# Kernel tuning notes

Hardware: AMD Instinct MI355X
Metric: run time of the kernel (lower is better)

Reference implementation:

```python
import jax, jax.numpy as jnp
import numpy as np

D_MODEL = 768
BATCH = 2
N_CTX = 4096


def setup_inputs() -> dict:
    key = jax.random.key(0)
    k1, k2 = jax.random.split(key)
    x = jax.random.normal(k1, (BATCH, N_CTX, D_MODEL), dtype=jnp.float32)
    # proj: Linear(d_model, 3*d_model, bias=False); torch stores weight as [out, in]
    W_proj = jax.random.normal(k2, (3 * D_MODEL, D_MODEL), dtype=jnp.float32) * (1.0 / np.sqrt(D_MODEL))
    return {"x": x, "W_proj": W_proj}


def reference(x, W_proj):
    d = x.shape[-1]
    n_ctx = x.shape[-2]
    # qkv: [B, S, 3D] = x @ W^T (torch Linear semantics)
    qkv = jnp.einsum("bsd,ed->bse", x, W_proj)
    Q, K, V = jnp.split(qkv, 3, axis=-1)
    # additive causal mask: 0 on/below diagonal, -inf above (1 - 1/tril(ones))
    causal = jnp.tril(jnp.ones((n_ctx, n_ctx), dtype=bool))
    mask = jnp.where(causal, 0.0, -jnp.inf).astype(x.dtype)
    # NOTE: no 1/sqrt(d) scaling in the original module
    scores = jnp.einsum("bqd,bkd->bqk", Q, K) + mask
    attn = jax.nn.softmax(scores, axis=-1)
    out = x + jnp.einsum("bqk,bkd->bqd", attn, V)
    return out
```

## Files before the change

### kernel.cpp

```cpp
#include <hip/hip_runtime.h>
#include <hip/hip_bf16.h>
#include <hip/hip_fp16.h>

typedef _Float16 f16;
typedef _Float16 f16x8 __attribute__((ext_vector_type(8)));
typedef _Float16 f16x4 __attribute__((ext_vector_type(4)));
typedef _Float16 f16x2 __attribute__((ext_vector_type(2)));
typedef float f32x4 __attribute__((ext_vector_type(4)));

#define D_MODEL 768
#define S_CTX   4096
#define NBATCH  2
#define M_TOK   (NBATCH * S_CTX)
#define N3      (3 * D_MODEL)

__device__ __forceinline__ void gload_lds16(const void* g, void* l) {
  __builtin_amdgcn_global_load_lds(
      (__attribute__((address_space(1))) unsigned int*)g,
      (__attribute__((address_space(3))) unsigned int*)l, 16, 0, 0);
}

__global__ __launch_bounds__(256) void cvt_f32_f16(const float* __restrict__ s,
                                                   f16* __restrict__ d, int n4) {
  int i = blockIdx.x * 256 + threadIdx.x;
  if (i >= n4) return;
  f32x4 v = ((const f32x4*)s)[i];
  f16x4 h;
  h[0] = (f16)v[0]; h[1] = (f16)v[1]; h[2] = (f16)v[2]; h[3] = (f16)v[3];
  ((f16x4*)d)[i] = h;
}

__global__ __launch_bounds__(256, 2) void proj_gemm(
    const f16* __restrict__ A, const f16* __restrict__ B,
    f16* __restrict__ qh, f16* __restrict__ kh, f16* __restrict__ vth) {
  __shared__ f16 As[128 * 32];
  __shared__ f16 Bs[128 * 32];

  const int tid  = threadIdx.x;
  const int w    = tid >> 6, lane = tid & 63;
  const int wr   = w >> 1,   wc   = w & 1;
  const int bm0  = blockIdx.x * 128, bn0 = blockIdx.y * 128;
  const int srow = lane >> 2;
  const int scol = (lane & 3) * 8;

  f32x4 acc[4][4] = {};

  const f16* gA = A + (size_t)bm0 * 768;
  const f16* gB = B + (size_t)bn0 * 768;

  for (int kt = 0; kt < 24; ++kt) {
    __syncthreads();
    const int k0 = kt * 32 + scol;
#pragma unroll
    for (int cc = 0; cc < 2; ++cc) {
      int c = w + cc * 4;
      gload_lds16(gA + (size_t)(c * 16 + srow) * 768 + k0, (char*)As + c * 1024);
      gload_lds16(gB + (size_t)(c * 16 + srow) * 768 + k0, (char*)Bs + c * 1024);
    }
    __syncthreads();

    const int fr = lane & 15, fk = (lane >> 4) * 8;
    f16x8 af[4], bf[4];
#pragma unroll
    for (int i = 0; i < 4; ++i)
      af[i] = *(const f16x8*)(As + (wr * 64 + i * 16 + fr) * 32 + fk);
#pragma unroll
    for (int j = 0; j < 4; ++j)
      bf[j] = *(const f16x8*)(Bs + (wc * 64 + j * 16 + fr) * 32 + fk);
#pragma unroll
    for (int i = 0; i < 4; ++i)
#pragma unroll
      for (int j = 0; j < 4; ++j)
        acc[i][j] = __builtin_amdgcn_mfma_f32_16x16x32_f16(af[i], bf[j], acc[i][j], 0, 0, 0);
  }

  const int fr = lane & 15, fq = lane >> 4;
#pragma unroll
  for (int i = 0; i < 4; ++i) {
#pragma unroll
    for (int j = 0; j < 4; ++j) {
      int gn      = bn0 + wc * 64 + j * 16 + fr;
      int gm_base = bm0 + wr * 64 + i * 16 + fq * 4;
      if (gn < 1536) {
        f16* dst = (gn < 768) ? qh : kh;
        int  col = (gn < 768) ? gn : gn - 768;
#pragma unroll
        for (int r = 0; r < 4; ++r)
          dst[(size_t)(gm_base + r) * 768 + col] = (f16)acc[i][j][r];
      } else {
        int d = gn - 1536;
        int bb = gm_base >> 12, s = gm_base & 4095;
        f16x4 h;
        h[0] = (f16)acc[i][j][0]; h[1] = (f16)acc[i][j][1];
        h[2] = (f16)acc[i][j][2]; h[3] = (f16)acc[i][j][3];
        *(f16x4*)(vth + ((size_t)bb * 768 + d) * 4096 + s) = h;
      }
    }
  }
}

#define SM_K0   0
#define SM_K1   49152
#define SM_SS   98304
#define SM_PS   106496
#define SM_M    108544
#define SM_L    108672
#define SM_F    108800
#define SM_SZ   108928

__global__ __launch_bounds__(512, 2) void attn_part(
    const f16* __restrict__ qg, const f16* __restrict__ kg,
    const f16* __restrict__ vt, f16* __restrict__ p0,
    float* __restrict__ p1, float* __restrict__ ml) {
  extern __shared__ __align__(16) char smem[];
  char*  Kb0 = smem + SM_K0;
  char*  Kb1 = smem + SM_K1;
  float* Ss0 = (float*)(smem + SM_SS);
  float* Ss1 = Ss0 + 1024;
  char*  Ps  = smem + SM_PS;
  float* mS  = (float*)(smem + SM_M);
  float* lS  = (float*)(smem + SM_L);
  float* fS  = (float*)(smem + SM_F);

  const int tid  = threadIdx.x;
  const int wv   = tid >> 6, lane = tid & 63;
  const int fr   = lane & 15, fq = lane >> 4;
  const int qi   = wv >> 2, ki = (wv >> 1) & 1, dh = wv & 1;

  const int u = blockIdx.x;
  int vv = (u < 256) ? u : (u - 256);
  const int qb = ((u < 256) ? 127 : 63) - (vv >> 2);
  const int b  = (vv >> 1) & 1;
  const int c  = vv & 1;
  const int q0 = qb * 32;
  const int n  = (q0 >> 5) + 1;
  const int n0 = (n + 1) >> 1;
  const int ts = c ? n0 : 0;
  const int te = c ? n : n0;

  const char* kbase = (const char*)(kg + (size_t)b * 4096 * 768);
  const f16*  vbase = vt + (size_t)b * 768 * 4096;
  const f16*  vp0   = vbase + (size_t)(wv * 96 + fr) * 4096 + fq * 8;

  f16x8 qreg[12];
  {
    const f16* qp = qg + ((size_t)b * 4096 + q0 + qi * 16 + fr) * 768 + dh * 384 + fq * 8;
#pragma unroll
    for (int kk = 0; kk < 12; ++kk) qreg[kk] = *(const f16x8*)(qp + kk * 32);
  }

  if (tid < 32) { mS[tid] = -1e30f; lS[tid] = 0.f; }

  f32x4 acc[2][6] = {};

  if (ts < te) {
    const char* kb = kbase + (size_t)(ts * 32) * 1536;
    char* dst = (ts & 1) ? Kb1 : Kb0;
#pragma unroll
    for (int i = 0; i < 6; ++i) {
      int lin = wv * 6144 + i * 1024 + lane * 16;
      int row = lin / 1536, cb = lin - row * 1536;
      gload_lds16(kb + (size_t)row * 1536 + (cb ^ ((row & 7) << 4)),
                  dst + wv * 6144 + i * 1024);
    }
  }
  asm volatile("s_waitcnt vmcnt(0)" ::: "memory");
  __builtin_amdgcn_s_barrier();

  for (int t = ts; t < te; ++t) {
    const int kv0 = t * 32;
    const bool pf = (t + 1 < te);

    f16x8 vreg[6];
    {
      const f16* vp = vp0 + kv0;
#pragma unroll
      for (int ct = 0; ct < 6; ++ct)
        vreg[ct] = *(const f16x8*)(vp + (size_t)ct * 16 * 4096);
    }
    if (pf) {
      const char* kb = kbase + (size_t)(kv0 + 32) * 1536;
      char* dst = ((t + 1) & 1) ? Kb1 : Kb0;
#pragma unroll
      for (int i = 0; i < 6; ++i) {
        int lin = wv * 6144 + i * 1024 + lane * 16;
        int row = lin / 1536, cb = lin - row * 1536;
        gload_lds16(kb + (size_t)row * 1536 + (cb ^ ((row & 7) << 4)),
                    dst + wv * 6144 + i * 1024);
      }
    }

    {
      const char* kbuf = (t & 1) ? Kb1 : Kb0;
      f32x4 sc = {};
      const int krow = ki * 16 + fr;
      const int kswz = (krow & 7) << 4;
      __builtin_amdgcn_s_setprio(1);
#pragma unroll
      for (int kk = 0; kk < 12; ++kk) {
        int by = krow * 1536 + dh * 768 + kk * 64 + fq * 16;
        f16x8 kf = *(const f16x8*)(kbuf + (by ^ kswz));
        sc = __builtin_amdgcn_mfma_f32_16x16x32_f16(qreg[kk], kf, sc, 0, 0, 0);
      }
      __builtin_amdgcn_s_setprio(0);
      float* sdst = (dh ? Ss1 : Ss0) + (qi * 16 + fq * 4) * 32 + ki * 16 + fr;
#pragma unroll
      for (int r = 0; r < 4; ++r) sdst[r * 32] = sc[r];
    }
    asm volatile("s_waitcnt lgkmcnt(0)" ::: "memory");
    __builtin_amdgcn_s_barrier();

    {
      const int row = tid >> 4, sub = tid & 15;
      const int c0 = sub * 2;
      float a0 = Ss0[row * 32 + c0]     + Ss1[row * 32 + c0];
      float a1 = Ss0[row * 32 + c0 + 1] + Ss1[row * 32 + c0 + 1];
      const int grow = q0 + row;
      if (kv0 + c0     > grow) a0 = -1e30f;
      if (kv0 + c0 + 1 > grow) a1 = -1e30f;
      float mx = fmaxf(a0, a1);
      mx = fmaxf(mx, __shfl_xor(mx, 1));
      mx = fmaxf(mx, __shfl_xor(mx, 2));
      mx = fmaxf(mx, __shfl_xor(mx, 4));
      mx = fmaxf(mx, __shfl_xor(mx, 8));
      float mo = mS[row];
      float mn = fmaxf(mo, mx);
      float p0v = __expf(a0 - mn), p1v = __expf(a1 - mn);
      float sum = p0v + p1v;
      sum += __shfl_xor(sum, 1);
      sum += __shfl_xor(sum, 2);
      sum += __shfl_xor(sum, 4);
      sum += __shfl_xor(sum, 8);
      if (sub == 0) {
        float f = __expf(mo - mn);
        mS[row] = mn; fS[row] = f; lS[row] = lS[row] * f + sum;
      }
      f16x2 ph; ph[0] = (f16)p0v; ph[1] = (f16)p1v;
      int by = row * 64 + sub * 4;
      *(f16x2*)(Ps + (by ^ (((row >> 1) & 3) << 4))) = ph;
    }
    asm volatile("s_waitcnt lgkmcnt(0)" ::: "memory");
    __builtin_amdgcn_s_barrier();

    {
      f32x4 f0 = *(const f32x4*)(fS + fq * 4);
      f32x4 f1 = *(const f32x4*)(fS + 16 + fq * 4);
#pragma unroll
      for (int ct = 0; ct < 6; ++ct)
#pragma unroll
        for (int r = 0; r < 4; ++r) {
          acc[0][ct][r] *= f0[r];
          acc[1][ct][r] *= f1[r];
        }
      int byA0 = (fr * 64 + fq * 16) ^ (((fr >> 1) & 3) << 4);
      int rb = 16 + fr;
      int byA1 = (rb * 64 + fq * 16) ^ (((rb >> 1) & 3) << 4);
      f16x8 pa0 = *(const f16x8*)(Ps + byA0);
      f16x8 pa1 = *(const f16x8*)(Ps + byA1);
      __builtin_amdgcn_s_setprio(1);
#pragma unroll
      for (int ct = 0; ct < 6; ++ct) {
        acc[0][ct] = __builtin_amdgcn_mfma_f32_16x16x32_f16(pa0, vreg[ct], acc[0][ct], 0, 0, 0);
        acc[1][ct] = __builtin_amdgcn_mfma_f32_16x16x32_f16(pa1, vreg[ct], acc[1][ct], 0, 0, 0);
      }
      __builtin_amdgcn_s_setprio(0);
    }
    asm volatile("s_waitcnt vmcnt(0) lgkmcnt(0)" ::: "memory");
    __builtin_amdgcn_s_barrier();
  }

  const size_t obase = (size_t)b * 4096 + q0;
  if (c == 0) {
#pragma unroll
    for (int ct = 0; ct < 6; ++ct) {
      int d = wv * 96 + ct * 16 + fr;
#pragma unroll
      for (int r = 0; r < 4; ++r) {
        p0[(obase + fq * 4 + r) * 768 + d]      = (f16)acc[0][ct][r];
        p0[(obase + 16 + fq * 4 + r) * 768 + d] = (f16)acc[1][ct][r];
      }
    }
  } else {
#pragma unroll
    for (int ct = 0; ct < 6; ++ct) {
      int d = wv * 96 + ct * 16 + fr;
#pragma unroll
      for (int r = 0; r < 4; ++r) {
        p1[(obase + fq * 4 + r) * 768 + d]      = acc[0][ct][r];
        p1[(obase + 16 + fq * 4 + r) * 768 + d] = acc[1][ct][r];
      }
    }
  }
  if (tid < 32) {
    float* mlp = ml + ((size_t)(c * 2 + b) * 4096 + q0 + tid) * 2;
    mlp[0] = mS[tid];
    mlp[1] = lS[tid];
  }
}

__global__ __launch_bounds__(256) void attn_combine(
    const float* __restrict__ x, const f16* __restrict__ p0,
    const float* __restrict__ ml, float* __restrict__ out) {
  int i = blockIdx.x * 256 + threadIdx.x;
  int row = i / 192;
  int b = row >> 12, s = row & 4095;
  const float* m0p = ml + ((size_t)b * 4096 + s) * 2;
  const float* m1p = ml + ((size_t)(2 + b) * 4096 + s) * 2;
  float m0 = m0p[0], l0 = m0p[1];
  float m1 = m1p[0], l1 = m1p[1];
  float m  = fmaxf(m0, m1);
  float f0 = __expf(m0 - m), f1 = __expf(m1 - m);
  float inv = 1.f / (l0 * f0 + l1 * f1);
  f32x4 a1 = ((const f32x4*)out)[i];
  f16x4 a0 = ((const f16x4*)p0)[i];
  f32x4 xv = ((const f32x4*)x)[i];
  f32x4 o;
#pragma unroll
  for (int r = 0; r < 4; ++r)
    o[r] = xv[r] + ((float)a0[r] * f0 + a1[r] * f1) * inv;
  ((f32x4*)out)[i] = o;
}

extern "C" void kernel_launch(void* const* d_in, const int* in_sizes, int n_in,
                              void* d_out, int out_size, void* d_ws, size_t ws_size,
                              hipStream_t stream) {
  const float* x  = (const float*)d_in[0];
  const float* Wp = (const float*)d_in[1];
  float* out = (float*)d_out;

  char* ws = (char*)d_ws;
  f16* x_h  = (f16*)(ws);
  f16* w_h  = (f16*)(ws + 12582912);
  f16* q_h  = (f16*)(ws + 16121856);
  f16* k_h  = (f16*)(ws + 28704768);
  f16* vt_h = (f16*)(ws + 41287680);

  f16*   p0 = x_h;
  float* ml = (float*)w_h;

  hipFuncSetAttribute(reinterpret_cast<const void*>(attn_part),
                      hipFuncAttributeMaxDynamicSharedMemorySize, SM_SZ);

  cvt_f32_f16<<<(M_TOK * D_MODEL) / 1024, 256, 0, stream>>>(x, x_h, (M_TOK * D_MODEL) / 4);
  cvt_f32_f16<<<(N3 * D_MODEL) / 1024, 256, 0, stream>>>(Wp, w_h, (N3 * D_MODEL) / 4);
  proj_gemm<<<dim3(64, 18), 256, 0, stream>>>(x_h, w_h, q_h, k_h, vt_h);
  attn_part<<<512, 512, SM_SZ, stream>>>(q_h, k_h, vt_h, p0, out, ml);
  attn_combine<<<(M_TOK * D_MODEL) / 1024, 256, 0, stream>>>(x, p0, ml, out);
}
```

Before: 284.2 us.

## Single-buffer K tile in LDS to allow four workgroups per CU

Replaces the double-buffered K tile with a single LDS buffer, roughly halving shared memory per block, and raises the launch-bounds occupancy hint from 2 to 4 blocks. The prefetch of the next K tile is now issued after the score barrier, so it overlaps only the softmax and PV phase rather than the whole iteration. The aim is to hide latency through more resident blocks instead of intra-block double buffering. The risks are register spilling under the tighter launch bound and less overlap within each block. A redundant reload of the current tile is issued on the last iteration.

```diff
diff --git a/kernel.cpp b/kernel.cpp
--- a/kernel.cpp
+++ b/kernel.cpp
@@ -99,22 +99,20 @@
   }
 }
 
-#define SM_K0   0
-#define SM_K1   49152
-#define SM_SS   98304
-#define SM_PS   106496
-#define SM_M    108544
-#define SM_L    108672
-#define SM_F    108800
-#define SM_SZ   108928
-
-__global__ __launch_bounds__(512, 2) void attn_part(
+#define SM_K    0
+#define SM_SS   49152
+#define SM_PS   57344
+#define SM_M    59392
+#define SM_L    59520
+#define SM_F    59648
+#define SM_SZ   59776
+
+__global__ __launch_bounds__(512, 4) void attn_part(
     const f16* __restrict__ qg, const f16* __restrict__ kg,
     const f16* __restrict__ vt, f16* __restrict__ p0,
     float* __restrict__ p1, float* __restrict__ ml) {
   extern __shared__ __align__(16) char smem[];
-  char*  Kb0 = smem + SM_K0;
-  char*  Kb1 = smem + SM_K1;
+  char*  Kb  = smem + SM_K;
   float* Ss0 = (float*)(smem + SM_SS);
   float* Ss1 = Ss0 + 1024;
   char*  Ps  = smem + SM_PS;
@@ -153,23 +151,24 @@
 
   f32x4 acc[2][6] = {};
 
-  if (ts < te) {
-    const char* kb = kbase + (size_t)(ts * 32) * 1536;
-    char* dst = (ts & 1) ? Kb1 : Kb0;
+  auto stageK = [&](int t) {
+    const char* kb = kbase + (size_t)(t * 32) * 1536;
 #pragma unroll
     for (int i = 0; i < 6; ++i) {
       int lin = wv * 6144 + i * 1024 + lane * 16;
       int row = lin / 1536, cb = lin - row * 1536;
       gload_lds16(kb + (size_t)row * 1536 + (cb ^ ((row & 7) << 4)),
-                  dst + wv * 6144 + i * 1024);
-    }
-  }
+                  Kb + wv * 6144 + i * 1024);
+    }
+  };
+
+  stageK(ts < te ? ts : 0);
   asm volatile("s_waitcnt vmcnt(0)" ::: "memory");
   __builtin_amdgcn_s_barrier();
 
   for (int t = ts; t < te; ++t) {
     const int kv0 = t * 32;
-    const bool pf = (t + 1 < te);
+    const int tn  = (t + 1 < te) ? t + 1 : t;
 
     f16x8 vreg[6];
     {
@@ -178,20 +177,8 @@
       for (int ct = 0; ct < 6; ++ct)
         vreg[ct] = *(const f16x8*)(vp + (size_t)ct * 16 * 4096);
     }
-    if (pf) {
-      const char* kb = kbase + (size_t)(kv0 + 32) * 1536;
-      char* dst = ((t + 1) & 1) ? Kb1 : Kb0;
-#pragma unroll
-      for (int i = 0; i < 6; ++i) {
-        int lin = wv * 6144 + i * 1024 + lane * 16;
-        int row = lin / 1536, cb = lin - row * 1536;
-        gload_lds16(kb + (size_t)row * 1536 + (cb ^ ((row & 7) << 4)),
-                    dst + wv * 6144 + i * 1024);
-      }
-    }
 
     {
-      const char* kbuf = (t & 1) ? Kb1 : Kb0;
       f32x4 sc = {};
       const int krow = ki * 16 + fr;
       const int kswz = (krow & 7) << 4;
@@ -199,7 +186,7 @@
 #pragma unroll
       for (int kk = 0; kk < 12; ++kk) {
         int by = krow * 1536 + dh * 768 + kk * 64 + fq * 16;
-        f16x8 kf = *(const f16x8*)(kbuf + (by ^ kswz));
+        f16x8 kf = *(const f16x8*)(Kb + (by ^ kswz));
         sc = __builtin_amdgcn_mfma_f32_16x16x32_f16(qreg[kk], kf, sc, 0, 0, 0);
       }
       __builtin_amdgcn_s_setprio(0);
@@ -209,6 +196,8 @@
     }
     asm volatile("s_waitcnt lgkmcnt(0)" ::: "memory");
     __builtin_amdgcn_s_barrier();
+
+    stageK(tn);
 
     {
       const int row = tid >> 4, sub = tid & 15;
```

New measurement: 672.7 us. 2.37x slower.
